# Kernel tuning notes

Measured on AMD Instinct MI355X. Metric: run time of the kernel, lower is better.

The kernel has to match this reference:

```python
import jax, jax.numpy as jnp
import numpy as np

B, N, D, K = 1024, 8192, 256, 8
LAMBDA_MULT = 0.01

def setup_inputs() -> dict:
    key = jax.random.key(0)
    k1, k2, k3, k4, k5 = jax.random.split(key, 5)
    x = jax.random.uniform(k1, (B, D), dtype=jnp.float32)
    mu = jax.random.uniform(k2, (N, D), dtype=jnp.float32)
    lambda_base = jax.random.uniform(k3, (N,), dtype=jnp.float32) * LAMBDA_MULT
    v = jax.random.normal(k4, (N, K, D), dtype=jnp.float32)  # stands in for per-unit orthogonal init
    omega = 0.1 + 0.4 * jax.random.uniform(k5, (N, K), dtype=jnp.float32)
    return {"x": x, "mu": mu, "lambda_base": lambda_base, "v": v, "omega": omega}

def reference(x, mu, lambda_base, v, omega):
    # quad_form = diff^T (lambda*I + sum_k omega_k v_k v_k^T) diff
    #           = lambda * ||x - mu||^2 + sum_k omega_k * ((x - mu) . v_k)^2
    # Woodbury-style expansion avoids materializing W:(n,d,d) and diff:(b,n,d).
    x2 = jnp.sum(x * x, axis=-1)                      # (b,)
    mu2 = jnp.sum(mu * mu, axis=-1)                   # (n,)
    xm = x @ mu.T                                     # (b,n)
    sqdist = x2[:, None] - 2.0 * xm + mu2[None, :]    # (b,n) = ||x-mu||^2
    xv = jnp.einsum('bd,nkd->bnk', x, v)              # (b,n,k)
    muv = jnp.einsum('nd,nkd->nk', mu, v)             # (n,k)
    proj2 = (xv - muv[None, :, :]) ** 2               # (b,n,k)
    quad = lambda_base[None, :] * sqdist + jnp.einsum('bnk,nk->bn', proj2, omega)
    return jnp.exp(-quad / D)  # Type == 'exp'
```

## Files before the change

kernel.cpp:

```cpp
#include <hip/hip_runtime.h>


#define B_SZ 1024
#define N_SZ 8192
#define D_SZ 256
#define K_SZ 8

#define BT 128
#define NT 16

typedef __bf16 bf16x8 __attribute__((ext_vector_type(8)));
typedef float f32x4 __attribute__((ext_vector_type(4)));
typedef unsigned short u16x4 __attribute__((ext_vector_type(4)));
typedef unsigned short u16x8 __attribute__((ext_vector_type(8)));

#define WS_X2   0u
#define WS_MU2  4096u
#define WS_MUV  36864u
#define WS_PX   299008u
#define WS_PW   823296u
#define WS_NEED (823296ull + 37748736ull)

__device__ __forceinline__ float wave_reduce(float s) {
#pragma unroll
  for (int off = 32; off > 0; off >>= 1) s += __shfl_down(s, off);
  return s;
}

__device__ __forceinline__ u16x4 cvt4(float4 t) {
  u16x4 r;
  r[0] = __builtin_bit_cast(unsigned short, (__bf16)t.x);
  r[1] = __builtin_bit_cast(unsigned short, (__bf16)t.y);
  r[2] = __builtin_bit_cast(unsigned short, (__bf16)t.z);
  r[3] = __builtin_bit_cast(unsigned short, (__bf16)t.w);
  return r;
}

__device__ __forceinline__ void glds16(const void* g, const void* l) {
  __builtin_amdgcn_global_load_lds(
      (const __attribute__((address_space(1))) void*)g,
      (__attribute__((address_space(3))) void*)l, 16, 0, 0);
}

__global__ void prep_all(const float* __restrict__ x, const float* __restrict__ mu,
                         const float* __restrict__ v,
                         float* __restrict__ x2, unsigned short* __restrict__ px,
                         float* __restrict__ mu2, float* __restrict__ muv,
                         unsigned short* __restrict__ pw) {
  const int w = threadIdx.x >> 6, lane = threadIdx.x & 63;
  const int g = blockIdx.x * 4 + w;
  if (g < B_SZ) {
    const int b = g;
    float4 t = *(const float4*)(x + (size_t)b * D_SZ + 4 * lane);
    *(u16x4*)(px + (size_t)b * D_SZ + 4 * lane) = cvt4(t);
    float s = t.x * t.x + t.y * t.y + t.z * t.z + t.w * t.w;
    s = wave_reduce(s);
    if (lane == 0) x2[b] = s;
  } else if (g < B_SZ + N_SZ) {
    const int n = g - B_SZ;
    float4 m4 = *(const float4*)(mu + (size_t)n * D_SZ + 4 * lane);
    *(u16x4*)(pw + (size_t)n * 9 * D_SZ + 4 * lane) = cvt4(m4);
    float s = m4.x * m4.x + m4.y * m4.y + m4.z * m4.z + m4.w * m4.w;
    s = wave_reduce(s);
    if (lane == 0) mu2[n] = s;
  } else {
    const int idx = g - (B_SZ + N_SZ);
    const int n = idx >> 3, k = idx & 7;
    float4 m4 = *(const float4*)(mu + (size_t)n * D_SZ + 4 * lane);
    float4 v4 = *(const float4*)(v + ((size_t)n * K_SZ + k) * D_SZ + 4 * lane);
    *(u16x4*)(pw + ((size_t)n * 9 + k + 1) * D_SZ + 4 * lane) = cvt4(v4);
    float s = m4.x * v4.x + m4.y * v4.y + m4.z * v4.z + m4.w * v4.w;
    s = wave_reduce(s);
    if (lane == 0) muv[n * K_SZ + k] = s;
  }
}

__device__ __forceinline__ void stage_tile(const unsigned short* __restrict__ px,
                                           const unsigned short* __restrict__ pw,
                                           unsigned short* As, unsigned short* Bs,
                                           int b0, int n0, int k0, int w, int lane) {
  const int nl4 = lane >> 2;
  const int ch = lane & 3;
  const int kc = (ch ^ ((nl4 >> 1) & 3)) * 8;
#pragma unroll
  for (int t = 0; t < 2; ++t) {
    int r0 = w * 32 + t * 16;
    glds16(px + (size_t)(b0 + r0 + nl4) * D_SZ + k0 + kc, As + r0 * 32);
  }
#pragma unroll
  for (int t = 0; t < 3; ++t) {
    int i = w + 4 * t;
    if (i < 9)
      glds16(pw + ((size_t)(n0 + nl4) * 9 + i) * D_SZ + k0 + kc, Bs + i * 16 * 32);
  }
}

__global__ __launch_bounds__(256, 2)
void hmu_main_p(const unsigned short* __restrict__ px,
                const unsigned short* __restrict__ pw,
                const float* __restrict__ lam, const float* __restrict__ om,
                const float* __restrict__ wsf, float* __restrict__ out) {
  __shared__ __align__(16) unsigned short As[BT * 32];
  __shared__ __align__(16) unsigned short Bs[NT * 9 * 32];

  const float* ws_x2 = wsf;
  const float* ws_mu2 = wsf + 1024;
  const float* ws_muv = wsf + 9216;

  const int tid = threadIdx.x;
  const int lane = tid & 63;
  const int w = tid >> 6;
  const int m = lane & 15;
  const int kg = lane >> 4;

  const int n0 = blockIdx.x * NT;
  const int b0 = blockIdx.y * BT;

  f32x4 acc[2][9];
#pragma unroll
  for (int bs = 0; bs < 2; ++bs)
#pragma unroll
    for (int j = 0; j < 9; ++j) acc[bs][j] = (f32x4){0.f, 0.f, 0.f, 0.f};

  const int sw = (kg ^ ((m >> 1) & 3)) * 8;

  for (int kt = 0; kt < 8; ++kt) {
    stage_tile(px, pw, As, Bs, b0, n0, kt * 32, w, lane);
    __syncthreads();

    bf16x8 af0 = *(const bf16x8*)&As[((2 * w + 0) * 16 + m) * 32 + sw];
    bf16x8 af1 = *(const bf16x8*)&As[((2 * w + 1) * 16 + m) * 32 + sw];
#pragma unroll
    for (int j = 0; j < 9; ++j) {
      bf16x8 bfr = *(const bf16x8*)&Bs[(j * 16 + m) * 32 + sw];
      acc[0][j] = __builtin_amdgcn_mfma_f32_16x16x32_bf16(af0, bfr, acc[0][j], 0, 0, 0);
      acc[1][j] = __builtin_amdgcn_mfma_f32_16x16x32_bf16(af1, bfr, acc[1][j], 0, 0, 0);
    }
    __syncthreads();
  }

  const int n = n0 + m;
  const float lam_n = lam[n];
  const float mu2_n = ws_mu2[n];
  float omr[8], muvr[8];
#pragma unroll
  for (int k = 0; k < 8; ++k) {
    omr[k] = om[n * 8 + k];
    muvr[k] = ws_muv[n * 8 + k];
  }
#pragma unroll
  for (int bs = 0; bs < 2; ++bs) {
#pragma unroll
    for (int r = 0; r < 4; ++r) {
      int b = b0 + (2 * w + bs) * 16 + kg * 4 + r;
      float x2b = ws_x2[b];
      float c0 = acc[bs][0][r];
      float q = lam_n * (x2b - 2.f * c0 + mu2_n);
#pragma unroll
      for (int k = 0; k < 8; ++k) {
        float p = acc[bs][k + 1][r] - muvr[k];
        q = fmaf(omr[k] * p, p, q);
      }
      out[(size_t)b * N_SZ + n] = __expf(q * (-1.0f / 256.0f));
    }
  }
}

__device__ __forceinline__ void cvt16_store(const float* __restrict__ src,
                                            unsigned short* dst) {
  const float4* p4 = (const float4*)src;
  float fv[16];
#pragma unroll
  for (int e = 0; e < 4; ++e) {
    float4 t = p4[e];
    fv[4 * e + 0] = t.x; fv[4 * e + 1] = t.y;
    fv[4 * e + 2] = t.z; fv[4 * e + 3] = t.w;
  }
  u16x8 lo, hi;
#pragma unroll
  for (int e = 0; e < 8; ++e) {
    lo[e] = __builtin_bit_cast(unsigned short, (__bf16)fv[e]);
    hi[e] = __builtin_bit_cast(unsigned short, (__bf16)fv[e + 8]);
  }
  *(u16x8*)dst = lo;
  *(u16x8*)(dst + 8) = hi;
}

#define LDS_STRIDE 40
__global__ __launch_bounds__(256, 2)
void hmu_main_f(const float* __restrict__ x, const float* __restrict__ mu,
                const float* __restrict__ lam, const float* __restrict__ v,
                const float* __restrict__ om, const float* __restrict__ ws,
                float* __restrict__ out) {
  __shared__ __align__(16) unsigned short As[BT * LDS_STRIDE];
  __shared__ __align__(16) unsigned short Bs[NT * 9 * LDS_STRIDE];
  const float* ws_x2 = ws;
  const float* ws_mu2 = ws + 1024;
  const float* ws_muv = ws + 9216;
  const int tid = threadIdx.x, lane = tid & 63, w = tid >> 6;
  const int m = lane & 15, kg = lane >> 4;
  const int n0 = blockIdx.x * NT, b0 = blockIdx.y * BT;
  f32x4 acc[2][9];
#pragma unroll
  for (int bs = 0; bs < 2; ++bs)
#pragma unroll
    for (int j = 0; j < 9; ++j) acc[bs][j] = (f32x4){0.f, 0.f, 0.f, 0.f};
  const int arow = tid >> 1, ahalf = tid & 1;
  for (int kt = 0; kt < 8; ++kt) {
    const int k0 = kt * 32;
    cvt16_store(x + (size_t)(b0 + arow) * D_SZ + k0 + ahalf * 16,
                &As[arow * LDS_STRIDE + ahalf * 16]);
#pragma unroll
    for (int it = 0; it < 2; ++it) {
      int idx = tid + 256 * it;
      if (idx < 288) {
        int row = idx >> 1, half = idx & 1;
        int nl = row / 9, j = row - nl * 9;
        const float* src = (j == 0)
            ? mu + (size_t)(n0 + nl) * D_SZ + k0 + half * 16
            : v + (size_t)((n0 + nl) * K_SZ + (j - 1)) * D_SZ + k0 + half * 16;
        cvt16_store(src, &Bs[row * LDS_STRIDE + half * 16]);
      }
    }
    __syncthreads();
    bf16x8 af[2];
#pragma unroll
    for (int bs = 0; bs < 2; ++bs)
      af[bs] = *(const bf16x8*)&As[((2 * w + bs) * 16 + m) * LDS_STRIDE + kg * 8];
#pragma unroll
    for (int j = 0; j < 9; ++j) {
      bf16x8 bfr = *(const bf16x8*)&Bs[(m * 9 + j) * LDS_STRIDE + kg * 8];
      acc[0][j] = __builtin_amdgcn_mfma_f32_16x16x32_bf16(af[0], bfr, acc[0][j], 0, 0, 0);
      acc[1][j] = __builtin_amdgcn_mfma_f32_16x16x32_bf16(af[1], bfr, acc[1][j], 0, 0, 0);
    }
    __syncthreads();
  }
  const int n = n0 + m;
  const float lam_n = lam[n];
  const float mu2_n = ws_mu2[n];
  float omr[8], muvr[8];
#pragma unroll
  for (int k = 0; k < 8; ++k) {
    omr[k] = om[n * 8 + k];
    muvr[k] = ws_muv[n * 8 + k];
  }
#pragma unroll
  for (int bs = 0; bs < 2; ++bs)
#pragma unroll
    for (int r = 0; r < 4; ++r) {
      int b = b0 + (2 * w + bs) * 16 + kg * 4 + r;
      float c0 = acc[bs][0][r];
      float q = lam_n * (ws_x2[b] - 2.f * c0 + mu2_n);
#pragma unroll
      for (int k = 0; k < 8; ++k) {
        float p = acc[bs][k + 1][r] - muvr[k];
        q = fmaf(omr[k] * p, p, q);
      }
      out[(size_t)b * N_SZ + n] = __expf(q * (-1.0f / 256.0f));
    }
}

__global__ void p2_mu_f(const float* __restrict__ mu, const float* __restrict__ v,
                        float* __restrict__ mu2, float* __restrict__ muv) {
  __shared__ __align__(16) float mulds[D_SZ];
  const int n = blockIdx.x;
  const int w = threadIdx.x >> 6, lane = threadIdx.x & 63;
  if (w == 0) {
    float4 m4 = *(const float4*)(mu + (size_t)n * D_SZ + 4 * lane);
    *(float4*)(mulds + 4 * lane) = m4;
    float s = m4.x * m4.x + m4.y * m4.y + m4.z * m4.z + m4.w * m4.w;
    s = wave_reduce(s);
    if (lane == 0) mu2[n] = s;
  }
  __syncthreads();
  float4 m4 = *(const float4*)(mulds + 4 * lane);
#pragma unroll
  for (int kk = 0; kk < 2; ++kk) {
    const int k = w * 2 + kk;
    float4 v4 = *(const float4*)(v + ((size_t)n * K_SZ + k) * D_SZ + 4 * lane);
    float s = m4.x * v4.x + m4.y * v4.y + m4.z * v4.z + m4.w * v4.w;
    s = wave_reduce(s);
    if (lane == 0) muv[n * K_SZ + k] = s;
  }
}

__global__ void p1_x2_f(const float* __restrict__ x, float* __restrict__ x2) {
  const int w = threadIdx.x >> 6, lane = threadIdx.x & 63;
  const int b = blockIdx.x * 4 + w;
  float4 t = *(const float4*)(x + (size_t)b * D_SZ + 4 * lane);
  float s = t.x * t.x + t.y * t.y + t.z * t.z + t.w * t.w;
  s = wave_reduce(s);
  if (lane == 0) x2[b] = s;
}

extern "C" void kernel_launch(void* const* d_in, const int* in_sizes, int n_in,
                              void* d_out, int out_size, void* d_ws, size_t ws_size,
                              hipStream_t stream) {
  const float* x   = (const float*)d_in[0];
  const float* mu  = (const float*)d_in[1];
  const float* lam = (const float*)d_in[2];
  const float* v   = (const float*)d_in[3];
  const float* om  = (const float*)d_in[4];
  float* out = (float*)d_out;
  char* wsb = (char*)d_ws;
  float* wsf = (float*)d_ws;
  float* x2  = (float*)(wsb + WS_X2);
  float* mu2 = (float*)(wsb + WS_MU2);
  float* muv = (float*)(wsb + WS_MUV);

  dim3 grid(N_SZ / NT, B_SZ / BT);
  if (ws_size >= WS_NEED) {
    unsigned short* px = (unsigned short*)(wsb + WS_PX);
    unsigned short* pw = (unsigned short*)(wsb + WS_PW);
    const int nunits = B_SZ + N_SZ + N_SZ * K_SZ;
    prep_all<<<nunits / 4, 256, 0, stream>>>(x, mu, v, x2, px, mu2, muv, pw);
    hmu_main_p<<<grid, 256, 0, stream>>>(px, pw, lam, om, wsf, out);
  } else {
    p1_x2_f<<<B_SZ / 4, 256, 0, stream>>>(x, x2);
    p2_mu_f<<<N_SZ, 256, 0, stream>>>(mu, v, mu2, muv);
    hmu_main_f<<<grid, 256, 0, stream>>>(x, mu, lam, v, om, wsf, out);
  }
}
```

Before: 172.6 us.

## Double-buffer LDS tiles with async prefetch and hoist epilogue loads

Splits the shared-memory A/B tiles into two buffers so the next K-slice is loaded directly to LDS while the current slice feeds the MFMAs. Per-wave vmcnt waits replace the full __syncthreads, and s_setprio raises wave priority during the MFMA block. The epilogue operands (lambda, mu2, omega, muv, x2) are now loaded before the main loop. In exchange the kernel uses twice the LDS and relies on hand-counted vmcnt values that must match the number of glds16 issues per wave.

Result: no change. 173.6 us (+0.6%).

```diff
diff --git a/kernel.cpp b/kernel.cpp
--- a/kernel.cpp
+++ b/kernel.cpp
@@ -100,8 +100,8 @@
                 const unsigned short* __restrict__ pw,
                 const float* __restrict__ lam, const float* __restrict__ om,
                 const float* __restrict__ wsf, float* __restrict__ out) {
-  __shared__ __align__(16) unsigned short As[BT * 32];
-  __shared__ __align__(16) unsigned short Bs[NT * 9 * 32];
+  __shared__ __align__(16) unsigned short As[2][BT * 32];
+  __shared__ __align__(16) unsigned short Bs[2][NT * 9 * 32];
 
   const float* ws_x2 = wsf;
   const float* ws_mu2 = wsf + 1024;
@@ -116,46 +116,69 @@
   const int n0 = blockIdx.x * NT;
   const int b0 = blockIdx.y * BT;
 
-  f32x4 acc[2][9];
-#pragma unroll
-  for (int bs = 0; bs < 2; ++bs)
-#pragma unroll
-    for (int j = 0; j < 9; ++j) acc[bs][j] = (f32x4){0.f, 0.f, 0.f, 0.f};
-
-  const int sw = (kg ^ ((m >> 1) & 3)) * 8;
-
-  for (int kt = 0; kt < 8; ++kt) {
-    stage_tile(px, pw, As, Bs, b0, n0, kt * 32, w, lane);
-    __syncthreads();
-
-    bf16x8 af0 = *(const bf16x8*)&As[((2 * w + 0) * 16 + m) * 32 + sw];
-    bf16x8 af1 = *(const bf16x8*)&As[((2 * w + 1) * 16 + m) * 32 + sw];
-#pragma unroll
-    for (int j = 0; j < 9; ++j) {
-      bf16x8 bfr = *(const bf16x8*)&Bs[(j * 16 + m) * 32 + sw];
-      acc[0][j] = __builtin_amdgcn_mfma_f32_16x16x32_bf16(af0, bfr, acc[0][j], 0, 0, 0);
-      acc[1][j] = __builtin_amdgcn_mfma_f32_16x16x32_bf16(af1, bfr, acc[1][j], 0, 0, 0);
-    }
-    __syncthreads();
-  }
-
   const int n = n0 + m;
   const float lam_n = lam[n];
   const float mu2_n = ws_mu2[n];
-  float omr[8], muvr[8];
+  float omr[8], muvr[8], x2r[2][4];
 #pragma unroll
   for (int k = 0; k < 8; ++k) {
     omr[k] = om[n * 8 + k];
     muvr[k] = ws_muv[n * 8 + k];
   }
 #pragma unroll
+  for (int bs = 0; bs < 2; ++bs)
+#pragma unroll
+    for (int r = 0; r < 4; ++r)
+      x2r[bs][r] = ws_x2[b0 + (2 * w + bs) * 16 + kg * 4 + r];
+  asm volatile("s_waitcnt vmcnt(0)" ::: "memory");
+
+  f32x4 acc[2][9];
+#pragma unroll
+  for (int bs = 0; bs < 2; ++bs)
+#pragma unroll
+    for (int j = 0; j < 9; ++j) acc[bs][j] = (f32x4){0.f, 0.f, 0.f, 0.f};
+
+  const int sw = (kg ^ ((m >> 1) & 3)) * 8;
+
+  stage_tile(px, pw, As[0], Bs[0], b0, n0, 0, w, lane);
+
+#pragma unroll
+  for (int kt = 0; kt < 8; ++kt) {
+    const int cur = kt & 1;
+    if (kt < 7) {
+      stage_tile(px, pw, As[cur ^ 1], Bs[cur ^ 1], b0, n0, (kt + 1) * 32, w, lane);
+      if (w == 0) asm volatile("s_waitcnt vmcnt(5)" ::: "memory");
+      else        asm volatile("s_waitcnt vmcnt(4)" ::: "memory");
+    } else {
+      asm volatile("s_waitcnt vmcnt(0)" ::: "memory");
+    }
+    __builtin_amdgcn_s_barrier();
+
+    const unsigned short* Ac = As[cur];
+    const unsigned short* Bc = Bs[cur];
+    bf16x8 af0 = *(const bf16x8*)&Ac[((2 * w + 0) * 16 + m) * 32 + sw];
+    bf16x8 af1 = *(const bf16x8*)&Ac[((2 * w + 1) * 16 + m) * 32 + sw];
+    __builtin_amdgcn_s_setprio(1);
+#pragma unroll
+    for (int j = 0; j < 9; ++j) {
+      bf16x8 bfr = *(const bf16x8*)&Bc[(j * 16 + m) * 32 + sw];
+      acc[0][j] = __builtin_amdgcn_mfma_f32_16x16x32_bf16(af0, bfr, acc[0][j], 0, 0, 0);
+      acc[1][j] = __builtin_amdgcn_mfma_f32_16x16x32_bf16(af1, bfr, acc[1][j], 0, 0, 0);
+    }
+    __builtin_amdgcn_s_setprio(0);
+    if (kt < 7) {
+      asm volatile("s_waitcnt lgkmcnt(0)" ::: "memory");
+      __builtin_amdgcn_s_barrier();
+    }
+  }
+
+#pragma unroll
   for (int bs = 0; bs < 2; ++bs) {
 #pragma unroll
     for (int r = 0; r < 4; ++r) {
       int b = b0 + (2 * w + bs) * 16 + kg * 4 + r;
-      float x2b = ws_x2[b];
       float c0 = acc[bs][0][r];
-      float q = lam_n * (x2b - 2.f * c0 + mu2_n);
+      float q = lam_n * (x2r[bs][r] - 2.f * c0 + mu2_n);
 #pragma unroll
       for (int k = 0; k < 8; ++k) {
         float p = acc[bs][k + 1][r] - muvr[k];
```

## Enlarge batch tile to 256 rows and remap blocks for XCD-local n reuse

Applied to the files above, without the earlier changes.

The main kernel's batch tile grows from 128 to 256 rows, with each wave computing four 16-row sub-blocks. The nine B fragments are loaded once per k-step and reused across all four row blocks, which halves how often the packed mu/v tile is loaded per output. A 1D grid with an XCD-aware block remap keeps the four batch tiles that share an n-tile on the same XCD, so their common weight data can hit in that XCD's L2. The cost is twice as many accumulator registers (36 f32x4) and a larger LDS footprint, which may lower occupancy below the launch bound of 2 blocks.

After: 162.3 us. -6.0%, faster.

```diff
diff --git a/kernel.cpp b/kernel.cpp
--- a/kernel.cpp
+++ b/kernel.cpp
@@ -6,6 +6,7 @@
 #define D_SZ 256
 #define K_SZ 8
 
+#define BTM 256
 #define BT 128
 #define NT 16
 
@@ -83,8 +84,8 @@
   const int ch = lane & 3;
   const int kc = (ch ^ ((nl4 >> 1) & 3)) * 8;
 #pragma unroll
-  for (int t = 0; t < 2; ++t) {
-    int r0 = w * 32 + t * 16;
+  for (int t = 0; t < 4; ++t) {
+    int r0 = w * 64 + t * 16;
     glds16(px + (size_t)(b0 + r0 + nl4) * D_SZ + k0 + kc, As + r0 * 32);
   }
 #pragma unroll
@@ -100,7 +101,7 @@
                 const unsigned short* __restrict__ pw,
                 const float* __restrict__ lam, const float* __restrict__ om,
                 const float* __restrict__ wsf, float* __restrict__ out) {
-  __shared__ __align__(16) unsigned short As[BT * 32];
+  __shared__ __align__(16) unsigned short As[BTM * 32];
   __shared__ __align__(16) unsigned short Bs[NT * 9 * 32];
 
   const float* ws_x2 = wsf;
@@ -113,14 +114,17 @@
   const int m = lane & 15;
   const int kg = lane >> 4;
 
-  const int n0 = blockIdx.x * NT;
-  const int b0 = blockIdx.y * BT;
-
-  f32x4 acc[2][9];
-#pragma unroll
-  for (int bs = 0; bs < 2; ++bs)
-#pragma unroll
-    for (int j = 0; j < 9; ++j) acc[bs][j] = (f32x4){0.f, 0.f, 0.f, 0.f};
+  const int bid = blockIdx.x;
+  const int xcd = bid & 7;
+  const int idx = bid >> 3;
+  const int n0 = (xcd * 64 + (idx >> 2)) * NT;
+  const int b0 = (idx & 3) * BTM;
+
+  f32x4 acc[4][9];
+#pragma unroll
+  for (int rb = 0; rb < 4; ++rb)
+#pragma unroll
+    for (int j = 0; j < 9; ++j) acc[rb][j] = (f32x4){0.f, 0.f, 0.f, 0.f};
 
   const int sw = (kg ^ ((m >> 1) & 3)) * 8;
 
@@ -128,13 +132,16 @@
     stage_tile(px, pw, As, Bs, b0, n0, kt * 32, w, lane);
     __syncthreads();
 
-    bf16x8 af0 = *(const bf16x8*)&As[((2 * w + 0) * 16 + m) * 32 + sw];
-    bf16x8 af1 = *(const bf16x8*)&As[((2 * w + 1) * 16 + m) * 32 + sw];
-#pragma unroll
-    for (int j = 0; j < 9; ++j) {
-      bf16x8 bfr = *(const bf16x8*)&Bs[(j * 16 + m) * 32 + sw];
-      acc[0][j] = __builtin_amdgcn_mfma_f32_16x16x32_bf16(af0, bfr, acc[0][j], 0, 0, 0);
-      acc[1][j] = __builtin_amdgcn_mfma_f32_16x16x32_bf16(af1, bfr, acc[1][j], 0, 0, 0);
+    bf16x8 bfr[9];
+#pragma unroll
+    for (int j = 0; j < 9; ++j)
+      bfr[j] = *(const bf16x8*)&Bs[(j * 16 + m) * 32 + sw];
+#pragma unroll
+    for (int rb = 0; rb < 4; ++rb) {
+      bf16x8 a = *(const bf16x8*)&As[((w * 4 + rb) * 16 + m) * 32 + sw];
+#pragma unroll
+      for (int j = 0; j < 9; ++j)
+        acc[rb][j] = __builtin_amdgcn_mfma_f32_16x16x32_bf16(a, bfr[j], acc[rb][j], 0, 0, 0);
     }
     __syncthreads();
   }
@@ -149,16 +156,16 @@
     muvr[k] = ws_muv[n * 8 + k];
   }
 #pragma unroll
-  for (int bs = 0; bs < 2; ++bs) {
+  for (int rb = 0; rb < 4; ++rb) {
 #pragma unroll
     for (int r = 0; r < 4; ++r) {
-      int b = b0 + (2 * w + bs) * 16 + kg * 4 + r;
+      int b = b0 + (w * 4 + rb) * 16 + kg * 4 + r;
       float x2b = ws_x2[b];
-      float c0 = acc[bs][0][r];
+      float c0 = acc[rb][0][r];
       float q = lam_n * (x2b - 2.f * c0 + mu2_n);
 #pragma unroll
       for (int k = 0; k < 8; ++k) {
-        float p = acc[bs][k + 1][r] - muvr[k];
+        float p = acc[rb][k + 1][r] - muvr[k];
         q = fmaf(omr[k] * p, p, q);
       }
       out[(size_t)b * N_SZ + n] = __expf(q * (-1.0f / 256.0f));
@@ -308,14 +315,14 @@
   float* mu2 = (float*)(wsb + WS_MU2);
   float* muv = (float*)(wsb + WS_MUV);
 
-  dim3 grid(N_SZ / NT, B_SZ / BT);
   if (ws_size >= WS_NEED) {
     unsigned short* px = (unsigned short*)(wsb + WS_PX);
     unsigned short* pw = (unsigned short*)(wsb + WS_PW);
     const int nunits = B_SZ + N_SZ + N_SZ * K_SZ;
     prep_all<<<nunits / 4, 256, 0, stream>>>(x, mu, v, x2, px, mu2, muv, pw);
-    hmu_main_p<<<grid, 256, 0, stream>>>(px, pw, lam, om, wsf, out);
+    hmu_main_p<<<(N_SZ / NT) * (B_SZ / BTM), 256, 0, stream>>>(px, pw, lam, om, wsf, out);
   } else {
+    dim3 grid(N_SZ / NT, B_SZ / BT);
     p1_x2_f<<<B_SZ / 4, 256, 0, stream>>>(x, x2);
     p2_mu_f<<<N_SZ, 256, 0, stream>>>(mu, v, mu2, muv);
     hmu_main_f<<<grid, 256, 0, stream>>>(x, mu, lam, v, om, wsf, out);
```
